# Optimization experiments

Measured on AMD Instinct MI355X. Metric: run time of the kernel, lower is better.

Reference implementation:

```python
import jax, jax.numpy as jnp
import numpy as np

WEIGHT = 1e-7       # lambda for the CRF loss
SIGMA_RGB = 15.0    # color-similarity bandwidth
SIGMA_XY = 100.0    # spatial-proximity bandwidth
SCALE = 0.5         # scale_factor (sigma_xy is multiplied by it in forward)


def setup_inputs() -> dict:
    key = jax.random.key(0)
    k1, k2 = jax.random.split(key)
    images = jax.random.uniform(k1, (4, 3, 128, 128), jnp.float32) * 255.0  # [0,255] RGB
    logits = jax.random.normal(k2, (4, 4, 128, 128), jnp.float32)
    segmentations = jax.nn.softmax(logits, axis=1)  # softmaxed logits, N*K*H*W
    return {"images": images, "segmentations": segmentations}


def _crf_loss(images, segmentations):
    n, k, h, w = segmentations.shape
    # F.interpolate(images, scale_factor=0.5, mode='nearest') == stride-2 subsample
    img_s = images[:, :, ::2, ::2]
    # F.interpolate(segs, scale_factor=0.5, mode='bilinear', align_corners=False)
    # for exact /2 downscale == 2x2 average pooling
    hs, ws = h // 2, w // 2
    seg_s = segmentations.reshape(n, k, hs, 2, ws, 2).mean(axis=(3, 5))  # [n,k,hs,ws]

    P = hs * ws
    yy, xx = jnp.meshgrid(jnp.arange(hs, dtype=jnp.float32),
                          jnp.arange(ws, dtype=jnp.float32), indexing='ij')
    sigma_xy_eff = SIGMA_XY * SCALE
    pos = jnp.stack([xx, yy], axis=-1).reshape(P, 2) / sigma_xy_eff      # [P,2]
    rgb = img_s.reshape(n, 3, P).transpose(0, 2, 1) / SIGMA_RGB          # [n,P,3]
    feats = jnp.concatenate([jnp.broadcast_to(pos[None], (n, P, 2)), rgb], axis=-1)  # [n,P,5]

    # exact dense Gaussian bilateral kernel W_ij = exp(-0.5*||f_i - f_j||^2)
    sq = jnp.sum(feats * feats, axis=-1)                                 # [n,P]
    d2 = sq[:, :, None] + sq[:, None, :] - 2.0 * jnp.einsum('npc,nqc->npq', feats, feats)
    Wk = jnp.exp(-0.5 * jnp.maximum(d2, 0.0))                            # [n,P,P]

    S = seg_s.reshape(n, k, P)
    AS = jnp.einsum('npq,nkq->nkp', Wk, S)                               # bilateral-filtered segs
    loss = -jnp.sum(S * AS) / jnp.float32(n)
    return (WEIGHT * loss).reshape(1)


def reference(images, segmentations):
    return _crf_loss(images, segmentations)
```

## Files before the change

### kernel.cpp

```cpp
#include <hip/hip_runtime.h>

#define NB    4
#define PPB   4096
#define BLK   256
#define NBLK2 2080
#define NPART (NBLK2 * NB)

#if __has_builtin(__builtin_amdgcn_exp2f)
#define EXPFN(x) __builtin_amdgcn_exp2f(x)
#define FSCALE 1.2011224087864498f
#else
#define EXPFN(x) __expf(x)
#define FSCALE 1.0f
#endif

typedef __attribute__((ext_vector_type(8))) short short8v;
typedef __attribute__((ext_vector_type(4))) float f32x4;

typedef unsigned int uint;
typedef unsigned short ushort;

__device__ __forceinline__ ushort bsplit(float v, float& rem) {
    uint u = __float_as_uint(v);
    uint r = (u + 0x7FFFu + ((u >> 16) & 1u)) >> 16;
    rem = v - __uint_as_float(r << 16);
    return (ushort)r;
}

__global__ __launch_bounds__(256) void crf_prep(const float* __restrict__ images,
                                                const float* __restrict__ segs,
                                                uint* __restrict__ FA,
                                                uint* __restrict__ FB,
                                                uint* __restrict__ SA,
                                                uint* __restrict__ SB,
                                                float* __restrict__ H) {
    int gid = blockIdx.x * BLK + threadIdx.x;
    int n = gid >> 12;
    int p = gid & (PPB - 1);
    int i = p >> 6;
    int j = p & 63;
    int off = 256 * i + 2 * j;
    const float* img = images + (size_t)n * 3 * 16384;
    float f[5];
    f[0] = (float)j * (FSCALE / 50.0f);
    f[1] = (float)i * (FSCALE / 50.0f);
    f[2] = img[off]         * (FSCALE / 15.0f);
    f[3] = img[16384 + off] * (FSCALE / 15.0f);
    f[4] = img[32768 + off] * (FSCALE / 15.0f);
    float h = -0.5f * (f[0]*f[0] + f[1]*f[1] + f[2]*f[2] + f[3]*f[3] + f[4]*f[4]);

    const float* sg = segs + (size_t)n * 4 * 16384;
    float s[4];
#pragma unroll
    for (int k = 0; k < 4; ++k) {
        float2 u0 = *(const float2*)(sg + k * 16384 + off);
        float2 u1 = *(const float2*)(sg + k * 16384 + off + 128);
        s[k] = 0.25f * ((u0.x + u0.y) + (u1.x + u1.y));
    }

    ushort v[3][5];
    ushort tg[2][4];
#pragma unroll
    for (int c = 0; c < 5; ++c) {
        float r1, r2, dead;
        v[0][c] = bsplit(f[c], r1);
        v[1][c] = bsplit(r1, r2);
        v[2][c] = bsplit(r2, dead);
    }
#pragma unroll
    for (int c = 0; c < 4; ++c) {
        float r1, dead;
        tg[0][c] = bsplit(s[c], r1);
        tg[1][c] = bsplit(r1, dead);
    }

    static const int PA[6] = {0, 0, 1, 0, 1, 2};
    static const int PB[6] = {0, 1, 0, 2, 1, 0};
    uint* fap = FA + (size_t)gid * 16;
    uint* fbp = FB + (size_t)gid * 16;
#pragma unroll
    for (int k2 = 0; k2 < 16; ++k2) {
        int s0 = 2 * k2, s1 = s0 + 1;
        uint lo = (s0 >= 30) ? 0u : (uint)v[PA[s0 / 5]][s0 % 5];
        uint hi = (s1 >= 30) ? 0u : (uint)v[PA[s1 / 5]][s1 % 5];
        fap[k2] = lo | (hi << 16);
        lo = (s0 >= 30) ? 0u : (uint)v[PB[s0 / 5]][s0 % 5];
        hi = (s1 >= 30) ? 0u : (uint)v[PB[s1 / 5]][s1 % 5];
        fbp[k2] = lo | (hi << 16);
    }
    static const int QA[3] = {0, 0, 1};
    static const int QB[3] = {0, 1, 0};
    uint* sap = SA + (size_t)gid * 16;
    uint* sbp = SB + (size_t)gid * 16;
#pragma unroll
    for (int k2 = 0; k2 < 16; ++k2) {
        int s0 = 2 * k2, s1 = s0 + 1;
        uint lo = (s0 >= 12) ? 0u : (uint)tg[QA[s0 / 4]][s0 % 4];
        uint hi = (s1 >= 12) ? 0u : (uint)tg[QA[s1 / 4]][s1 % 4];
        sap[k2] = lo | (hi << 16);
        lo = (s0 >= 12) ? 0u : (uint)tg[QB[s0 / 4]][s0 % 4];
        hi = (s1 >= 12) ? 0u : (uint)tg[QB[s1 / 4]][s1 % 4];
        sbp[k2] = lo | (hi << 16);
    }
    H[gid] = h;
}

__global__ __launch_bounds__(256, 6) void crf_pairs(const uint4* __restrict__ FA,
                                                    const uint4* __restrict__ FB,
                                                    const uint4* __restrict__ SA,
                                                    const uint4* __restrict__ SB,
                                                    const float* __restrict__ H,
                                                    float* __restrict__ part) {
    __shared__ float wsum[BLK / 64];
    int t = threadIdx.x;
    int n = blockIdx.y;
    int lane = t & 63;
    int w = t >> 6;
    int l15 = lane & 15;
    int lhi = lane >> 4;

    int b = blockIdx.x;
    int pc = 0;
#pragma unroll
    for (int i = 1; i < 64; ++i) pc += (b >= (64 * i - (i * (i - 1)) / 2)) ? 1 : 0;
    int qc = b - (64 * pc - (pc * (pc - 1)) / 2) + pc;
    bool diagblk = (pc == qc);
    int base = n << 12;
    int prow0 = pc * 64 + w * 16;

    size_t arow = (size_t)(base + prow0 + l15) * 4 + lhi;
    short8v afrag = __builtin_bit_cast(short8v, FA[arow]);
    short8v safrag = __builtin_bit_cast(short8v, SA[arow]);
    float hp[4];
#pragma unroll
    for (int r = 0; r < 4; ++r)
        hp[r] = H[base + prow0 + lhi * 4 + r];

    float accP = 0.f;
    float accD = 0.f;

#pragma unroll
    for (int jj = 0; jj < 4; ++jj) {
        if (diagblk && jj < w) continue;
        int qrow0 = qc * 64 + jj * 16;
        size_t brow = (size_t)(base + qrow0 + l15) * 4 + lhi;
        short8v bfrag = __builtin_bit_cast(short8v, FB[brow]);
        short8v sbfrag = __builtin_bit_cast(short8v, SB[brow]);
        float hq = H[base + qrow0 + l15];

        f32x4 cf = {0.f, 0.f, 0.f, 0.f};
        f32x4 cs = {0.f, 0.f, 0.f, 0.f};
        cf = __builtin_amdgcn_mfma_f32_16x16x32_bf16(afrag, bfrag, cf, 0, 0, 0);
        cs = __builtin_amdgcn_mfma_f32_16x16x32_bf16(safrag, sbfrag, cs, 0, 0, 0);

        if (diagblk && jj == w) {
#pragma unroll
            for (int r = 0; r < 4; ++r) {
                float d = cf[r] + (hp[r] + hq);
                float wg = EXPFN(d);
                int pg = lhi * 4 + r;
                float fw = (l15 > pg) ? 2.0f : ((l15 == pg) ? 1.0f : 0.0f);
                accD = fmaf(wg * fw, cs[r], accD);
            }
        } else {
#pragma unroll
            for (int r = 0; r < 4; ++r) {
                float d = cf[r] + (hp[r] + hq);
                float wg = EXPFN(d);
                accP = fmaf(wg, cs[r], accP);
            }
        }
    }

    float acc_all = 2.0f * accP + accD;
#pragma unroll
    for (int off = 32; off > 0; off >>= 1)
        acc_all += __shfl_down(acc_all, off, 64);
    if ((t & 63) == 0) wsum[t >> 6] = acc_all;
    __syncthreads();
    if (t == 0) {
        part[n * NBLK2 + blockIdx.x] =
            (wsum[0] + wsum[1]) + (wsum[2] + wsum[3]);
    }
}

__global__ __launch_bounds__(256) void crf_reduce(const float* __restrict__ part,
                                                  float* __restrict__ out) {
    __shared__ float wsum[BLK / 64];
    int t = threadIdx.x;
    float s = 0.f;
#pragma unroll
    for (int i = 0; i < 33; ++i) {
        int idx = t + i * BLK;
        if (idx < NPART) s += part[idx];
    }
#pragma unroll
    for (int off = 32; off > 0; off >>= 1)
        s += __shfl_down(s, off, 64);
    if ((t & 63) == 0) wsum[t >> 6] = s;
    __syncthreads();
    if (t == 0) {
        float tot = (wsum[0] + wsum[1]) + (wsum[2] + wsum[3]);
        out[0] = tot * (-2.5e-8f);
    }
}

extern "C" void kernel_launch(void* const* d_in, const int* in_sizes, int n_in,
                              void* d_out, int out_size, void* d_ws, size_t ws_size,
                              hipStream_t stream) {
    const float* images = (const float*)d_in[0];
    const float* segs   = (const float*)d_in[1];
    float* out = (float*)d_out;
    char* ws = (char*)d_ws;
    uint* FA = (uint*)(ws);
    uint* FB = (uint*)(ws + (1u << 20));
    uint* SA = (uint*)(ws + (2u << 20));
    uint* SB = (uint*)(ws + (3u << 20));
    float* H = (float*)(ws + (4u << 20));
    float* part = (float*)(ws + (4u << 20) + 65536);
    (void)in_sizes; (void)n_in; (void)out_size; (void)ws_size;

    crf_prep<<<dim3(64), dim3(256), 0, stream>>>(images, segs, FA, FB, SA, SB, H);
    crf_pairs<<<dim3(NBLK2, NB), dim3(256), 0, stream>>>(
        (const uint4*)FA, (const uint4*)FB, (const uint4*)SA, (const uint4*)SB, H, part);
    crf_reduce<<<dim3(1), dim3(256), 0, stream>>>(part, out);
}
```

Baseline: 87.25 us.

## Enlarge pair tiles to 128x128 with two A fragments per wave

The pair kernel now covers 128x128 upper-triangular tiles instead of 64x64. Each wave holds two 16-row A fragments and reuses every loaded B fragment for two MFMA pairs, which cuts the block count and B/H reloads per pair. The prep kernel also writes its packed bf16 split features as uint4 vector stores instead of scalar stores. In exchange, register use goes up (launch bound lowered to 4), there are fewer blocks for load balancing, and diagonal tiles waste more work because of masking.

Result: faster. 80.41 us (-7.8%).

```diff
diff --git a/kernel.cpp b/kernel.cpp
--- a/kernel.cpp
+++ b/kernel.cpp
@@ -3,8 +3,10 @@
 #define NB    4
 #define PPB   4096
 #define BLK   256
-#define NBLK2 2080
-#define NPART (NBLK2 * NB)
+#define CHK   128
+#define NCHK  32
+#define NBLK3 528
+#define NPART (NBLK3 * NB)
 
 #if __has_builtin(__builtin_amdgcn_exp2f)
 #define EXPFN(x) __builtin_amdgcn_exp2f(x)
@@ -76,36 +78,45 @@
 
     static const int PA[6] = {0, 0, 1, 0, 1, 2};
     static const int PB[6] = {0, 1, 0, 2, 1, 0};
-    uint* fap = FA + (size_t)gid * 16;
-    uint* fbp = FB + (size_t)gid * 16;
+    uint fa[16], fb[16], sa[16], sb[16];
 #pragma unroll
     for (int k2 = 0; k2 < 16; ++k2) {
         int s0 = 2 * k2, s1 = s0 + 1;
         uint lo = (s0 >= 30) ? 0u : (uint)v[PA[s0 / 5]][s0 % 5];
         uint hi = (s1 >= 30) ? 0u : (uint)v[PA[s1 / 5]][s1 % 5];
-        fap[k2] = lo | (hi << 16);
+        fa[k2] = lo | (hi << 16);
         lo = (s0 >= 30) ? 0u : (uint)v[PB[s0 / 5]][s0 % 5];
         hi = (s1 >= 30) ? 0u : (uint)v[PB[s1 / 5]][s1 % 5];
-        fbp[k2] = lo | (hi << 16);
+        fb[k2] = lo | (hi << 16);
     }
     static const int QA[3] = {0, 0, 1};
     static const int QB[3] = {0, 1, 0};
-    uint* sap = SA + (size_t)gid * 16;
-    uint* sbp = SB + (size_t)gid * 16;
 #pragma unroll
     for (int k2 = 0; k2 < 16; ++k2) {
         int s0 = 2 * k2, s1 = s0 + 1;
         uint lo = (s0 >= 12) ? 0u : (uint)tg[QA[s0 / 4]][s0 % 4];
         uint hi = (s1 >= 12) ? 0u : (uint)tg[QA[s1 / 4]][s1 % 4];
-        sap[k2] = lo | (hi << 16);
+        sa[k2] = lo | (hi << 16);
         lo = (s0 >= 12) ? 0u : (uint)tg[QB[s0 / 4]][s0 % 4];
         hi = (s1 >= 12) ? 0u : (uint)tg[QB[s1 / 4]][s1 % 4];
-        sbp[k2] = lo | (hi << 16);
+        sb[k2] = lo | (hi << 16);
+    }
+
+    uint4* fap = (uint4*)(FA + (size_t)gid * 16);
+    uint4* fbp = (uint4*)(FB + (size_t)gid * 16);
+    uint4* sap = (uint4*)(SA + (size_t)gid * 16);
+    uint4* sbp = (uint4*)(SB + (size_t)gid * 16);
+#pragma unroll
+    for (int k = 0; k < 4; ++k) {
+        fap[k] = make_uint4(fa[4*k], fa[4*k+1], fa[4*k+2], fa[4*k+3]);
+        fbp[k] = make_uint4(fb[4*k], fb[4*k+1], fb[4*k+2], fb[4*k+3]);
+        sap[k] = make_uint4(sa[4*k], sa[4*k+1], sa[4*k+2], sa[4*k+3]);
+        sbp[k] = make_uint4(sb[4*k], sb[4*k+1], sb[4*k+2], sb[4*k+3]);
     }
     H[gid] = h;
 }
 
-__global__ __launch_bounds__(256, 6) void crf_pairs(const uint4* __restrict__ FA,
+__global__ __launch_bounds__(256, 4) void crf_pairs(const uint4* __restrict__ FA,
                                                     const uint4* __restrict__ FB,
                                                     const uint4* __restrict__ SA,
                                                     const uint4* __restrict__ SB,
@@ -122,52 +133,64 @@
     int b = blockIdx.x;
     int pc = 0;
 #pragma unroll
-    for (int i = 1; i < 64; ++i) pc += (b >= (64 * i - (i * (i - 1)) / 2)) ? 1 : 0;
-    int qc = b - (64 * pc - (pc * (pc - 1)) / 2) + pc;
+    for (int i = 1; i < NCHK; ++i) pc += (b >= (i * (2 * NCHK + 1 - i)) / 2) ? 1 : 0;
+    int qc = b - (pc * (2 * NCHK + 1 - pc)) / 2 + pc;
     bool diagblk = (pc == qc);
     int base = n << 12;
-    int prow0 = pc * 64 + w * 16;
-
-    size_t arow = (size_t)(base + prow0 + l15) * 4 + lhi;
-    short8v afrag = __builtin_bit_cast(short8v, FA[arow]);
-    short8v safrag = __builtin_bit_cast(short8v, SA[arow]);
-    float hp[4];
-#pragma unroll
-    for (int r = 0; r < 4; ++r)
-        hp[r] = H[base + prow0 + lhi * 4 + r];
+    int prow0 = pc * CHK + w * 32;
+
+    size_t ar = (size_t)(base + prow0 + l15) * 4 + lhi;
+    short8v a0  = __builtin_bit_cast(short8v, FA[ar]);
+    short8v a1  = __builtin_bit_cast(short8v, FA[ar + 64]);
+    short8v sa0 = __builtin_bit_cast(short8v, SA[ar]);
+    short8v sa1 = __builtin_bit_cast(short8v, SA[ar + 64]);
+    float hp0[4], hp1[4];
+#pragma unroll
+    for (int r = 0; r < 4; ++r) {
+        hp0[r] = H[base + prow0 + lhi * 4 + r];
+        hp1[r] = H[base + prow0 + 16 + lhi * 4 + r];
+    }
 
     float accP = 0.f;
     float accD = 0.f;
 
 #pragma unroll
-    for (int jj = 0; jj < 4; ++jj) {
-        if (diagblk && jj < w) continue;
-        int qrow0 = qc * 64 + jj * 16;
-        size_t brow = (size_t)(base + qrow0 + l15) * 4 + lhi;
-        short8v bfrag = __builtin_bit_cast(short8v, FB[brow]);
-        short8v sbfrag = __builtin_bit_cast(short8v, SB[brow]);
+    for (int jj = 0; jj < 8; ++jj) {
+        if (diagblk && jj < 2 * w) continue;
+        int qrow0 = qc * CHK + jj * 16;
+        size_t br = (size_t)(base + qrow0 + l15) * 4 + lhi;
+        short8v bf  = __builtin_bit_cast(short8v, FB[br]);
+        short8v sbf = __builtin_bit_cast(short8v, SB[br]);
         float hq = H[base + qrow0 + l15];
 
-        f32x4 cf = {0.f, 0.f, 0.f, 0.f};
-        f32x4 cs = {0.f, 0.f, 0.f, 0.f};
-        cf = __builtin_amdgcn_mfma_f32_16x16x32_bf16(afrag, bfrag, cf, 0, 0, 0);
-        cs = __builtin_amdgcn_mfma_f32_16x16x32_bf16(safrag, sbfrag, cs, 0, 0, 0);
-
-        if (diagblk && jj == w) {
+        f32x4 cf0 = {0.f, 0.f, 0.f, 0.f};
+        f32x4 cf1 = {0.f, 0.f, 0.f, 0.f};
+        f32x4 cs0 = {0.f, 0.f, 0.f, 0.f};
+        f32x4 cs1 = {0.f, 0.f, 0.f, 0.f};
+        cf0 = __builtin_amdgcn_mfma_f32_16x16x32_bf16(a0, bf, cf0, 0, 0, 0);
+        cf1 = __builtin_amdgcn_mfma_f32_16x16x32_bf16(a1, bf, cf1, 0, 0, 0);
+        cs0 = __builtin_amdgcn_mfma_f32_16x16x32_bf16(sa0, sbf, cs0, 0, 0, 0);
+        cs1 = __builtin_amdgcn_mfma_f32_16x16x32_bf16(sa1, sbf, cs1, 0, 0, 0);
+
+        if (!diagblk) {
 #pragma unroll
             for (int r = 0; r < 4; ++r) {
-                float d = cf[r] + (hp[r] + hq);
-                float wg = EXPFN(d);
-                int pg = lhi * 4 + r;
-                float fw = (l15 > pg) ? 2.0f : ((l15 == pg) ? 1.0f : 0.0f);
-                accD = fmaf(wg * fw, cs[r], accD);
+                accP = fmaf(EXPFN(cf0[r] + (hp0[r] + hq)), cs0[r], accP);
+                accP = fmaf(EXPFN(cf1[r] + (hp1[r] + hq)), cs1[r], accP);
             }
         } else {
+            int qgb = qrow0 + l15;
+            int pgb = prow0 + lhi * 4;
 #pragma unroll
             for (int r = 0; r < 4; ++r) {
-                float d = cf[r] + (hp[r] + hq);
-                float wg = EXPFN(d);
-                accP = fmaf(wg, cs[r], accP);
+                float w0 = EXPFN(cf0[r] + (hp0[r] + hq));
+                int pg0 = pgb + r;
+                float f0 = (qgb > pg0) ? 2.0f : ((qgb == pg0) ? 1.0f : 0.0f);
+                accD = fmaf(w0 * f0, cs0[r], accD);
+                float w1 = EXPFN(cf1[r] + (hp1[r] + hq));
+                int pg1 = pg0 + 16;
+                float f1 = (qgb > pg1) ? 2.0f : ((qgb == pg1) ? 1.0f : 0.0f);
+                accD = fmaf(w1 * f1, cs1[r], accD);
             }
         }
     }
@@ -179,7 +202,7 @@
     if ((t & 63) == 0) wsum[t >> 6] = acc_all;
     __syncthreads();
     if (t == 0) {
-        part[n * NBLK2 + blockIdx.x] =
+        part[n * NBLK3 + blockIdx.x] =
             (wsum[0] + wsum[1]) + (wsum[2] + wsum[3]);
     }
 }
@@ -190,7 +213,7 @@
     int t = threadIdx.x;
     float s = 0.f;
 #pragma unroll
-    for (int i = 0; i < 33; ++i) {
+    for (int i = 0; i < 9; ++i) {
         int idx = t + i * BLK;
         if (idx < NPART) s += part[idx];
     }
@@ -221,7 +244,7 @@
     (void)in_sizes; (void)n_in; (void)out_size; (void)ws_size;
 
     crf_prep<<<dim3(64), dim3(256), 0, stream>>>(images, segs, FA, FB, SA, SB, H);
-    crf_pairs<<<dim3(NBLK2, NB), dim3(256), 0, stream>>>(
+    crf_pairs<<<dim3(NBLK3, NB), dim3(256), 0, stream>>>(
         (const uint4*)FA, (const uint4*)FB, (const uint4*)SA, (const uint4*)SB, H, part);
     crf_reduce<<<dim3(1), dim3(256), 0, stream>>>(part, out);
 }
```
